# Optimization experiments

Measured on AMD Instinct MI355X. Metric: run time of the kernel, lower is better.

## Reference

```python
import jax, jax.numpy as jnp
import numpy as np

GRID_SIZE = 8
POS_LAMBDA = 250.0
POS_MARGIN = 1.0
NEG_MARGIN = 0.2
N, C, H, W = 2, 256, 48, 64


def setup_inputs() -> dict:
    key = jax.random.key(0)
    k1, k2, k3 = jax.random.split(key, 3)
    desc1 = jax.random.normal(k1, (N, C, H, W), dtype=jnp.float32)
    desc2 = jax.random.normal(k2, (N, C, H, W), dtype=jnp.float32)
    # near-identity homography so the warp stays well-conditioned
    homo = jnp.eye(3, dtype=jnp.float32) + 0.01 * jax.random.normal(k3, (3, 3), dtype=jnp.float32)
    return {"desc1": desc1, "desc2": desc2, "homo": homo}


def _create_grid(n, h, w, dtype):
    # cell-center pixel coordinates, (x, y) order in the last dim
    gy, gx = jnp.meshgrid(jnp.arange(h, dtype=dtype), jnp.arange(w, dtype=dtype), indexing="ij")
    g = jnp.stack([gx, gy], axis=-1) * GRID_SIZE + GRID_SIZE // 2  # [h, w, 2]
    return jnp.broadcast_to(g, (n, h, w, 2))


def _warp_grid(grid, homo):
    ones = jnp.ones(grid.shape[:-1] + (1,), grid.dtype)
    pts = jnp.concatenate([grid, ones], axis=-1)          # [n, h, w, 3]
    wp = jnp.einsum("nhwc,rc->nhwr", pts, homo)           # apply H to homogeneous pts
    return wp[..., :2] / wp[..., 2:3]


def reference(desc1, desc2, homo):
    n, c, h, w = desc1.shape
    grid = _create_grid(n, h, w, desc1.dtype)             # [n, h, w, 2]
    w_grid = _warp_grid(grid, homo)                       # [n, h, w, 2]
    # all-pairs distance between source cell centers and warped cell centers
    diff = grid[:, :, :, None, None, :] - w_grid[:, None, None, :, :, :]  # [n,h,w,h,w,2]
    grid_dist = jnp.linalg.norm(diff, axis=-1)            # [n, h, w, h, w]
    s = (grid_dist <= GRID_SIZE - 0.5).astype(desc1.dtype)
    # dense all-pairs descriptor correlation (contraction over C)
    dot_desc = jnp.einsum("nchw,ncij->nhwij", desc1, desc2)  # [n, h, w, h, w]
    pos_dist = jnp.maximum(POS_MARGIN - dot_desc, 0.0)
    neg_dist = jnp.maximum(dot_desc - NEG_MARGIN, 0.0)
    loss = POS_LAMBDA * s * pos_dist + (1.0 - s) * neg_dist
    return loss.mean()
```

## Files before the change

kernel.cpp:

```cpp
#include <hip/hip_runtime.h>


#define GS 8
#define POS_LAMBDA 250.0f
#define POS_MARGIN 1.0f
#define NEG_MARGIN 0.2f
#define N_ 2
#define C_ 256
#define H_ 48
#define W_ 64
#define P_ (H_ * W_)
#define R2_THRESH 56.25f

#define BM 128
#define BN 192
#define BK 64
#define TM (P_ / BM)
#define TN (P_ / BN)
#define GEMM_BLOCKS (N_ * TM * TN)
#define ANBYTES 16384
#define BNBYTES 24576

typedef __attribute__((ext_vector_type(8))) short short8;
typedef __attribute__((ext_vector_type(4))) float floatx4;

__device__ __forceinline__ unsigned short f32_to_bf16(float f) {
    unsigned u = __builtin_bit_cast(unsigned, f);
    unsigned r = (u + 0x7FFFu + ((u >> 16) & 1u)) >> 16;
    return (unsigned short)r;
}

__device__ __forceinline__ void load16_to_lds(const void* g, void* l) {
    __builtin_amdgcn_global_load_lds(
        (const __attribute__((address_space(1))) void*)g,
        (__attribute__((address_space(3))) void*)l, 16, 0, 0);
}

__global__ __launch_bounds__(256) void prep_kernel(const float* __restrict__ in1,
                                                   const float* __restrict__ in2,
                                                   const float* __restrict__ homo,
                                                   unsigned short* __restrict__ o1,
                                                   unsigned short* __restrict__ o2,
                                                   float* __restrict__ wg) {
    int bid = blockIdx.x;
    int t = threadIdx.x;

    if (bid < 12) {
        int p = bid * 256 + t;
        float gx = (float)((p & (W_ - 1)) * GS + GS / 2);
        float gy = (float)((p >> 6) * GS + GS / 2);
        float h0 = homo[0], h1 = homo[1], h2 = homo[2];
        float h3 = homo[3], h4 = homo[4], h5 = homo[5];
        float h6 = homo[6], h7 = homo[7], h8 = homo[8];
        float w0 = fmaf(h0, gx, fmaf(h1, gy, h2));
        float w1 = fmaf(h3, gx, fmaf(h4, gy, h5));
        float w2 = fmaf(h6, gx, fmaf(h7, gy, h8));
        wg[2 * p]     = w0 / w2;
        wg[2 * p + 1] = w1 / w2;
        return;
    }

    int b = bid - 12;
    int d = b & 1;
    int r = b >> 1;
    int n = r / (48 * 4);
    int r2 = r % (48 * 4);
    int pt = r2 >> 2;
    int ct = r2 & 3;
    const float* src = (d ? in2 : in1) + ((size_t)n * C_ + ct * 64) * P_ + pt * 64;
    unsigned short* dst = (d ? o2 : o1) + ((size_t)n * P_ + (size_t)pt * 64) * C_ + ct * 64;

    __shared__ unsigned short tile[64][64];

#pragma unroll
    for (int i = 0; i < 4; ++i) {
        int idx = t + i * 256;
        int c = idx >> 4;
        int p4 = (idx & 15) << 2;
        float4 v = *(const float4*)(src + (size_t)c * P_ + p4);
        float vv[4] = {v.x, v.y, v.z, v.w};
#pragma unroll
        for (int rr = 0; rr < 4; ++rr) {
            int p = p4 + rr;
            int sw = (p & 7) ^ ((p >> 3) & 7);
            int slot = (c >> 3) ^ sw;
            tile[p][slot * 8 + (c & 7)] = f32_to_bf16(vv[rr]);
        }
    }
    __syncthreads();
#pragma unroll
    for (int i = 0; i < 2; ++i) {
        int idx = t + i * 256;
        int p = idx >> 3;
        int c8 = idx & 7;
        int sw = (p & 7) ^ ((p >> 3) & 7);
        short8 val = *(const short8*)&tile[p][(c8 ^ sw) * 8];
        *(short8*)(dst + (size_t)p * C_ + c8 * 8) = val;
    }
}

__global__ __launch_bounds__(256, 3) void mfma_hinge_kernel(const unsigned short* __restrict__ bf1,
                                                            const unsigned short* __restrict__ bf2,
                                                            const float* __restrict__ wg,
                                                            const float* __restrict__ homo,
                                                            float* __restrict__ partial) {
    __shared__ __attribute__((aligned(16))) char smem[ANBYTES + BNBYTES];

    const int bid = (blockIdx.x & 7) * (GEMM_BLOCKS / 8) + (blockIdx.x >> 3);
    const int n   = bid / (TM * TN);
    const int rem = bid % (TM * TN);
    const int bp1 = (rem / TN) * BM;
    const int bp2 = (rem % TN) * BN;
    const unsigned short* A = bf1 + (size_t)n * P_ * C_;
    const unsigned short* B = bf2 + (size_t)n * P_ * C_;

    const int t    = threadIdx.x;
    const int lane = t & 63;
    const int wv   = t >> 6;
    const int wr   = wv >> 1;
    const int wc   = wv & 1;
    const int sub  = lane >> 3;
    const int slot = lane & 7;
    const int c16  = slot ^ sub;

    bool skip;
    {
        float h3 = homo[3], h4 = homo[4], h5 = homo[5];
        float h6 = homo[6], h7 = homo[7], h8 = homo[8];
        float y2a = (float)((bp2 >> 6) * GS + GS / 2);
        float y2b = y2a + 16.0f;
        float wymin = 1e30f, wymax = -1e30f;
        bool ok = true;
#pragma unroll
        for (int cidx = 0; cidx < 4; ++cidx) {
            float x = (cidx & 1) ? 508.0f : 4.0f;
            float y = (cidx & 2) ? y2b : y2a;
            float w2 = fmaf(h6, x, fmaf(h7, y, h8));
            ok = ok && (w2 > 1e-6f);
            float wy = fmaf(h3, x, fmaf(h4, y, h5)) / w2;
            wymin = fminf(wymin, wy);
            wymax = fmaxf(wymax, wy);
        }
        float y1min = (float)((bp1 >> 6) * GS + GS / 2);
        float y1max = y1min + 8.0f;
        skip = ok && ((y1max < wymin - 7.6f) || (y1min > wymax + 7.6f));
    }

    floatx4 acc[4][6];
#pragma unroll
    for (int i = 0; i < 4; ++i)
#pragma unroll
        for (int j = 0; j < 6; ++j)
            acc[i][j] = floatx4{0.0f, 0.0f, 0.0f, 0.0f};

    for (int k0 = 0; k0 < C_; k0 += BK) {
        if (k0) __syncthreads();
#pragma unroll
        for (int i = 0; i < 4; ++i) {
            int chunk = wv * 4 + i;
            int row = chunk * 8 + sub;
            load16_to_lds((const char*)(A + (size_t)(bp1 + row) * C_ + k0) + c16 * 16,
                          smem + chunk * 1024);
        }
#pragma unroll
        for (int i = 0; i < 6; ++i) {
            int chunk = wv * 6 + i;
            int row = chunk * 8 + sub;
            load16_to_lds((const char*)(B + (size_t)(bp2 + row) * C_ + k0) + c16 * 16,
                          smem + ANBYTES + chunk * 1024);
        }
        __syncthreads();

#pragma unroll
        for (int kk = 0; kk < 2; ++kk) {
            short8 af[4], bfr[6];
#pragma unroll
            for (int i = 0; i < 4; ++i) {
                int row = wr * 64 + i * 16 + (lane & 15);
                int q   = kk * 4 + (lane >> 4);
                int off = row * 128 + ((q ^ (row & 7)) << 4);
                af[i] = *(const short8*)(smem + off);
            }
#pragma unroll
            for (int j = 0; j < 6; ++j) {
                int row = wc * 96 + j * 16 + (lane & 15);
                int q   = kk * 4 + (lane >> 4);
                int off = row * 128 + ((q ^ (row & 7)) << 4);
                bfr[j] = *(const short8*)(smem + ANBYTES + off);
            }
#pragma unroll
            for (int i = 0; i < 4; ++i)
#pragma unroll
                for (int j = 0; j < 6; ++j)
                    acc[i][j] = __builtin_amdgcn_mfma_f32_16x16x32_bf16(af[i], bfr[j],
                                                                        acc[i][j], 0, 0, 0);
        }
    }

    const int col   = lane & 15;
    const int rbase = (lane >> 4) * 4;
    float lsum = 0.0f;
    if (skip) {
#pragma unroll
        for (int j = 0; j < 6; ++j)
#pragma unroll
            for (int i = 0; i < 4; ++i)
#pragma unroll
                for (int r = 0; r < 4; ++r)
                    lsum += fmaxf(acc[i][j][r] - NEG_MARGIN, 0.0f);
    } else {
#pragma unroll
        for (int j = 0; j < 6; ++j) {
            int p2 = bp2 + wc * 96 + j * 16 + col;
            float wx = wg[2 * p2], wy = wg[2 * p2 + 1];
#pragma unroll
            for (int i = 0; i < 4; ++i) {
                int p1b = bp1 + wr * 64 + i * 16 + rbase;
#pragma unroll
                for (int r = 0; r < 4; ++r) {
                    int p1 = p1b + r;
                    float gx = (float)((p1 & (W_ - 1)) * GS + GS / 2);
                    float gy = (float)((p1 >> 6) * GS + GS / 2);
                    float dx = gx - wx, dy = gy - wy;
                    float r2 = fmaf(dx, dx, dy * dy);
                    float dot = acc[i][j][r];
                    float pos = fmaxf(POS_MARGIN - dot, 0.0f);
                    float neg = fmaxf(dot - NEG_MARGIN, 0.0f);
                    lsum += (r2 <= R2_THRESH) ? POS_LAMBDA * pos : neg;
                }
            }
        }
    }

#pragma unroll
    for (int off = 32; off > 0; off >>= 1)
        lsum += __shfl_down(lsum, off, 64);

    float* red = (float*)smem;
    if (lane == 0) red[wv] = lsum;
    __syncthreads();
    if (t == 0) partial[bid] = red[0] + red[1] + red[2] + red[3];
}

__global__ __launch_bounds__(256) void reduce_kernel(const float* __restrict__ partial,
                                                     float* __restrict__ out) {
    __shared__ double sd[256];
    int t = threadIdx.x;
    double s = 0.0;
    for (int i = t; i < GEMM_BLOCKS; i += 256) s += (double)partial[i];
    sd[t] = s;
    __syncthreads();
    for (int off = 128; off > 0; off >>= 1) {
        if (t < off) sd[t] += sd[t + off];
        __syncthreads();
    }
    if (t == 0) {
        double cnt = (double)N_ * (double)P_ * (double)P_;
        out[0] = (float)(sd[0] / cnt);
    }
}

extern "C" void kernel_launch(void* const* d_in, const int* in_sizes, int n_in,
                              void* d_out, int out_size, void* d_ws, size_t ws_size,
                              hipStream_t stream) {
    const float* desc1 = (const float*)d_in[0];
    const float* desc2 = (const float*)d_in[1];
    const float* homo  = (const float*)d_in[2];
    float* out = (float*)d_out;

    unsigned short* b1 = (unsigned short*)d_ws;
    unsigned short* b2 = b1 + (size_t)N_ * P_ * C_;
    float* partial = (float*)(b2 + (size_t)N_ * P_ * C_);
    float* wgbuf   = partial + GEMM_BLOCKS;

    prep_kernel<<<780, 256, 0, stream>>>(desc1, desc2, homo, b1, b2, wgbuf);
    mfma_hinge_kernel<<<GEMM_BLOCKS, 256, 0, stream>>>(b1, b2, wgbuf, homo, partial);
    reduce_kernel<<<1, 256, 0, stream>>>(partial, out);
}
```

Measured before the change: 28.19 us.

## Double-buffer LDS tiles with async global-to-LDS prefetch two stages ahead

Halves the K step to 32 and splits shared memory into two buffers so the direct global-to-LDS loads for later K slices are issued while MFMAs run on the current slice. Explicit vmcnt waits and raw barriers replace the full __syncthreads per step, and the LDS swizzle is reworked for the 64-byte row pitch. The aim is to hide global load latency in this short K=256 GEMM. The cost is more barriers per K step and fewer MFMAs between them, with some risk that the hand-written waitcnt counts are subtly wrong.

```diff
diff --git a/kernel.cpp b/kernel.cpp
--- a/kernel.cpp
+++ b/kernel.cpp
@@ -14,12 +14,14 @@
 
 #define BM 128
 #define BN 192
-#define BK 64
+#define BK 32
+#define NKS (C_ / BK)
 #define TM (P_ / BM)
 #define TN (P_ / BN)
 #define GEMM_BLOCKS (N_ * TM * TN)
-#define ANBYTES 16384
-#define BNBYTES 24576
+#define ABYTES 8192
+#define BBYTES 12288
+#define BUFB (ABYTES + BBYTES)
 
 typedef __attribute__((ext_vector_type(8))) short short8;
 typedef __attribute__((ext_vector_type(4))) float floatx4;
@@ -104,7 +106,7 @@
                                                             const float* __restrict__ wg,
                                                             const float* __restrict__ homo,
                                                             float* __restrict__ partial) {
-    __shared__ __attribute__((aligned(16))) char smem[ANBYTES + BNBYTES];
+    __shared__ __attribute__((aligned(16))) char smem[2 * BUFB];
 
     const int bid = (blockIdx.x & 7) * (GEMM_BLOCKS / 8) + (blockIdx.x >> 3);
     const int n   = bid / (TM * TN);
@@ -119,9 +121,71 @@
     const int wv   = t >> 6;
     const int wr   = wv >> 1;
     const int wc   = wv & 1;
-    const int sub  = lane >> 3;
-    const int slot = lane & 7;
-    const int c16  = slot ^ sub;
+
+    const int srow = lane >> 2;
+    const int sc16 = (lane & 3) ^ ((lane >> 3) & 3);
+    const int rslot = ((lane >> 4) ^ ((lane >> 1) & 3)) << 4;
+
+    floatx4 acc[4][6];
+#pragma unroll
+    for (int i = 0; i < 4; ++i)
+#pragma unroll
+        for (int j = 0; j < 6; ++j)
+            acc[i][j] = floatx4{0.0f, 0.0f, 0.0f, 0.0f};
+
+#define STAGE(off, k0)                                                               \
+    do {                                                                             \
+        _Pragma("unroll")                                                            \
+        for (int i_ = 0; i_ < 2; ++i_) {                                             \
+            int chunk = wv * 2 + i_;                                                 \
+            int row = chunk * 16 + srow;                                             \
+            load16_to_lds((const char*)(A + (size_t)(bp1 + row) * C_ + (k0)) + sc16 * 16, \
+                          smem + (off) + chunk * 1024);                              \
+        }                                                                            \
+        _Pragma("unroll")                                                            \
+        for (int i_ = 0; i_ < 3; ++i_) {                                             \
+            int chunk = wv * 3 + i_;                                                 \
+            int row = chunk * 16 + srow;                                             \
+            load16_to_lds((const char*)(B + (size_t)(bp2 + row) * C_ + (k0)) + sc16 * 16, \
+                          smem + (off) + ABYTES + chunk * 1024);                     \
+        }                                                                            \
+    } while (0)
+
+    STAGE(0, 0);
+    STAGE(BUFB, BK);
+
+#pragma unroll
+    for (int k = 0; k < NKS; ++k) {
+        if (k < NKS - 1) asm volatile("s_waitcnt vmcnt(5)" ::: "memory");
+        else             asm volatile("s_waitcnt vmcnt(0)" ::: "memory");
+        __builtin_amdgcn_s_barrier();
+
+        const char* cur = smem + (size_t)(k & 1) * BUFB;
+        short8 af[4], bfr[6];
+#pragma unroll
+        for (int i = 0; i < 4; ++i) {
+            int row = wr * 64 + i * 16 + (lane & 15);
+            af[i] = *(const short8*)(cur + row * 64 + rslot);
+        }
+#pragma unroll
+        for (int j = 0; j < 6; ++j) {
+            int row = wc * 96 + j * 16 + (lane & 15);
+            bfr[j] = *(const short8*)(cur + ABYTES + row * 64 + rslot);
+        }
+#pragma unroll
+        for (int i = 0; i < 4; ++i)
+#pragma unroll
+            for (int j = 0; j < 6; ++j)
+                acc[i][j] = __builtin_amdgcn_mfma_f32_16x16x32_bf16(af[i], bfr[j],
+                                                                    acc[i][j], 0, 0, 0);
+
+        asm volatile("s_waitcnt lgkmcnt(0)" ::: "memory");
+        __builtin_amdgcn_sched_barrier(0);
+        __builtin_amdgcn_s_barrier();
+
+        if (k < NKS - 2) STAGE((size_t)(k & 1) * BUFB, (k + 2) * BK);
+    }
+#undef STAGE
 
     bool skip;
     {
@@ -144,57 +208,6 @@
         float y1min = (float)((bp1 >> 6) * GS + GS / 2);
         float y1max = y1min + 8.0f;
         skip = ok && ((y1max < wymin - 7.6f) || (y1min > wymax + 7.6f));
-    }
-
-    floatx4 acc[4][6];
-#pragma unroll
-    for (int i = 0; i < 4; ++i)
-#pragma unroll
-        for (int j = 0; j < 6; ++j)
-            acc[i][j] = floatx4{0.0f, 0.0f, 0.0f, 0.0f};
-
-    for (int k0 = 0; k0 < C_; k0 += BK) {
-        if (k0) __syncthreads();
-#pragma unroll
-        for (int i = 0; i < 4; ++i) {
-            int chunk = wv * 4 + i;
-            int row = chunk * 8 + sub;
-            load16_to_lds((const char*)(A + (size_t)(bp1 + row) * C_ + k0) + c16 * 16,
-                          smem + chunk * 1024);
-        }
-#pragma unroll
-        for (int i = 0; i < 6; ++i) {
-            int chunk = wv * 6 + i;
-            int row = chunk * 8 + sub;
-            load16_to_lds((const char*)(B + (size_t)(bp2 + row) * C_ + k0) + c16 * 16,
-                          smem + ANBYTES + chunk * 1024);
-        }
-        __syncthreads();
-
-#pragma unroll
-        for (int kk = 0; kk < 2; ++kk) {
-            short8 af[4], bfr[6];
-#pragma unroll
-            for (int i = 0; i < 4; ++i) {
-                int row = wr * 64 + i * 16 + (lane & 15);
-                int q   = kk * 4 + (lane >> 4);
-                int off = row * 128 + ((q ^ (row & 7)) << 4);
-                af[i] = *(const short8*)(smem + off);
-            }
-#pragma unroll
-            for (int j = 0; j < 6; ++j) {
-                int row = wc * 96 + j * 16 + (lane & 15);
-                int q   = kk * 4 + (lane >> 4);
-                int off = row * 128 + ((q ^ (row & 7)) << 4);
-                bfr[j] = *(const short8*)(smem + ANBYTES + off);
-            }
-#pragma unroll
-            for (int i = 0; i < 4; ++i)
-#pragma unroll
-                for (int j = 0; j < 6; ++j)
-                    acc[i][j] = __builtin_amdgcn_mfma_f32_16x16x32_bf16(af[i], bfr[j],
-                                                                        acc[i][j], 0, 0, 0);
-        }
     }
 
     const int col   = lane & 15;
```

Result: slower. 31.25 us (+10.9%).

## Load MFMA operands directly from global memory instead of staging through LDS

Applied to the files above, without the earlier changes.

Drops the LDS-staged tiling (global_load_lds plus swizzled LDS reads and barriers) and has each wave load its bf16 A and B fragments straight from global memory into registers, fully unrolled over K. This removes the LDS traffic and the __syncthreads per K-step. In exchange each wave fetches its own rows, so operands shared across waves are read several times through the cache hierarchy rather than once. The change also drops the occupancy hint from launch bounds, which may raise register use.

```diff
diff --git a/kernel.cpp b/kernel.cpp
--- a/kernel.cpp
+++ b/kernel.cpp
@@ -14,12 +14,9 @@
 
 #define BM 128
 #define BN 192
-#define BK 64
 #define TM (P_ / BM)
 #define TN (P_ / BN)
 #define GEMM_BLOCKS (N_ * TM * TN)
-#define ANBYTES 16384
-#define BNBYTES 24576
 
 typedef __attribute__((ext_vector_type(8))) short short8;
 typedef __attribute__((ext_vector_type(4))) float floatx4;
@@ -28,12 +25,6 @@
     unsigned u = __builtin_bit_cast(unsigned, f);
     unsigned r = (u + 0x7FFFu + ((u >> 16) & 1u)) >> 16;
     return (unsigned short)r;
-}
-
-__device__ __forceinline__ void load16_to_lds(const void* g, void* l) {
-    __builtin_amdgcn_global_load_lds(
-        (const __attribute__((address_space(1))) void*)g,
-        (__attribute__((address_space(3))) void*)l, 16, 0, 0);
 }
 
 __global__ __launch_bounds__(256) void prep_kernel(const float* __restrict__ in1,
@@ -99,13 +90,11 @@
     }
 }
 
-__global__ __launch_bounds__(256, 3) void mfma_hinge_kernel(const unsigned short* __restrict__ bf1,
-                                                            const unsigned short* __restrict__ bf2,
-                                                            const float* __restrict__ wg,
-                                                            const float* __restrict__ homo,
-                                                            float* __restrict__ partial) {
-    __shared__ __attribute__((aligned(16))) char smem[ANBYTES + BNBYTES];
-
+__global__ __launch_bounds__(256) void mfma_hinge_kernel(const unsigned short* __restrict__ bf1,
+                                                         const unsigned short* __restrict__ bf2,
+                                                         const float* __restrict__ wg,
+                                                         const float* __restrict__ homo,
+                                                         float* __restrict__ partial) {
     const int bid = (blockIdx.x & 7) * (GEMM_BLOCKS / 8) + (blockIdx.x >> 3);
     const int n   = bid / (TM * TN);
     const int rem = bid % (TM * TN);
@@ -119,9 +108,35 @@
     const int wv   = t >> 6;
     const int wr   = wv >> 1;
     const int wc   = wv & 1;
-    const int sub  = lane >> 3;
-    const int slot = lane & 7;
-    const int c16  = slot ^ sub;
+
+    const unsigned short* Abase =
+        A + (size_t)(bp1 + wr * 64 + (lane & 15)) * C_ + (lane >> 4) * 8;
+    const unsigned short* Bbase =
+        B + (size_t)(bp2 + wc * 96 + (lane & 15)) * C_ + (lane >> 4) * 8;
+
+    floatx4 acc[4][6];
+#pragma unroll
+    for (int i = 0; i < 4; ++i)
+#pragma unroll
+        for (int j = 0; j < 6; ++j)
+            acc[i][j] = floatx4{0.0f, 0.0f, 0.0f, 0.0f};
+
+#pragma unroll
+    for (int s = 0; s < C_ / 32; ++s) {
+        short8 af[4], bfr[6];
+#pragma unroll
+        for (int i = 0; i < 4; ++i)
+            af[i] = *(const short8*)(Abase + (size_t)i * 16 * C_ + s * 32);
+#pragma unroll
+        for (int j = 0; j < 6; ++j)
+            bfr[j] = *(const short8*)(Bbase + (size_t)j * 16 * C_ + s * 32);
+#pragma unroll
+        for (int i = 0; i < 4; ++i)
+#pragma unroll
+            for (int j = 0; j < 6; ++j)
+                acc[i][j] = __builtin_amdgcn_mfma_f32_16x16x32_bf16(af[i], bfr[j],
+                                                                    acc[i][j], 0, 0, 0);
+    }
 
     bool skip;
     {
@@ -144,57 +159,6 @@
         float y1min = (float)((bp1 >> 6) * GS + GS / 2);
         float y1max = y1min + 8.0f;
         skip = ok && ((y1max < wymin - 7.6f) || (y1min > wymax + 7.6f));
-    }
-
-    floatx4 acc[4][6];
-#pragma unroll
-    for (int i = 0; i < 4; ++i)
-#pragma unroll
-        for (int j = 0; j < 6; ++j)
-            acc[i][j] = floatx4{0.0f, 0.0f, 0.0f, 0.0f};
-
-    for (int k0 = 0; k0 < C_; k0 += BK) {
-        if (k0) __syncthreads();
-#pragma unroll
-        for (int i = 0; i < 4; ++i) {
-            int chunk = wv * 4 + i;
-            int row = chunk * 8 + sub;
-            load16_to_lds((const char*)(A + (size_t)(bp1 + row) * C_ + k0) + c16 * 16,
-                          smem + chunk * 1024);
-        }
-#pragma unroll
-        for (int i = 0; i < 6; ++i) {
-            int chunk = wv * 6 + i;
-            int row = chunk * 8 + sub;
-            load16_to_lds((const char*)(B + (size_t)(bp2 + row) * C_ + k0) + c16 * 16,
-                          smem + ANBYTES + chunk * 1024);
-        }
-        __syncthreads();
-
-#pragma unroll
-        for (int kk = 0; kk < 2; ++kk) {
-            short8 af[4], bfr[6];
-#pragma unroll
-            for (int i = 0; i < 4; ++i) {
-                int row = wr * 64 + i * 16 + (lane & 15);
-                int q   = kk * 4 + (lane >> 4);
-                int off = row * 128 + ((q ^ (row & 7)) << 4);
-                af[i] = *(const short8*)(smem + off);
-            }
-#pragma unroll
-            for (int j = 0; j < 6; ++j) {
-                int row = wc * 96 + j * 16 + (lane & 15);
-                int q   = kk * 4 + (lane >> 4);
-                int off = row * 128 + ((q ^ (row & 7)) << 4);
-                bfr[j] = *(const short8*)(smem + ANBYTES + off);
-            }
-#pragma unroll
-            for (int i = 0; i < 4; ++i)
-#pragma unroll
-                for (int j = 0; j < 6; ++j)
-                    acc[i][j] = __builtin_amdgcn_mfma_f32_16x16x32_bf16(af[i], bfr[j],
-                                                                        acc[i][j], 0, 0, 0);
-        }
     }
 
     const int col   = lane & 15;
@@ -236,7 +200,7 @@
     for (int off = 32; off > 0; off >>= 1)
         lsum += __shfl_down(lsum, off, 64);
 
-    float* red = (float*)smem;
+    __shared__ float red[4];
     if (lane == 0) red[wv] = lsum;
     __syncthreads();
     if (t == 0) partial[bid] = red[0] + red[1] + red[2] + red[3];
```

After: 51.05 us. +81.1%, slower.
